# Kernel tuning notes

Hardware: AMD Instinct MI355X
Metric: run time of the kernel (lower is better)

## Reference

```python
import jax, jax.numpy as jnp
import numpy as np
import math

CH = 512
HEADS = 8
GROUPS = 32
EPS = 1e-5


def group_norm(x, w, b):
    # x: [B, C, T]
    B, C, T = x.shape
    xg = x.reshape(B, GROUPS, C // GROUPS, T)
    mu = xg.mean(axis=(2, 3), keepdims=True)
    var = xg.var(axis=(2, 3), keepdims=True)
    xg = (xg - mu) * jax.lax.rsqrt(var + EPS)
    return xg.reshape(B, C, T) * w[None, :, None] + b[None, :, None]


def conv1x1(x, w, b):
    # x: [B, C, T], w: [O, C, 1]
    return jnp.einsum('oc,bct->bot', w[:, :, 0], x) + b[None, :, None]


def conv3_same(x, w, b):
    y = jax.lax.conv_general_dilated(x, w, window_strides=(1,), padding='SAME',
                                     dimension_numbers=('NCH', 'OIH', 'NCH'))
    return y + b[None, :, None]


def setup_inputs() -> dict:
    key = jax.random.key(0)
    ks = jax.random.split(key, 12)
    B, Ti, Ts = 2, 4096, 1024
    inp = {
        'image': jax.random.normal(ks[0], (B, Ti, CH), jnp.float32),
        'st': jax.random.normal(ks[1], (B, Ts, CH), jnp.float32),
        'xn_w': jnp.ones((CH,), jnp.float32),
        'xn_b': jnp.zeros((CH,), jnp.float32),
        'jn_w': jnp.ones((CH,), jnp.float32),
        'jn_b': jnp.zeros((CH,), jnp.float32),
        'xqkv_w': jax.random.normal(ks[2], (3 * CH, CH, 1), jnp.float32) * (1.0 / math.sqrt(CH)),
        'xqkv_b': jnp.zeros((3 * CH,), jnp.float32),
        'jqkv_w': jax.random.normal(ks[3], (3 * CH, CH, 1), jnp.float32) * (1.0 / math.sqrt(CH)),
        'jqkv_b': jnp.zeros((3 * CH,), jnp.float32),
        # NOTE: original zero-inits proj; we use small random weights so the
        # attention path contributes to the output (same math).
        'proj_w': jax.random.normal(ks[4], (CH, CH, 3), jnp.float32) * (0.02 / math.sqrt(3 * CH)),
        'proj_b': jnp.zeros((CH,), jnp.float32),
    }
    return inp


def reference(image, st, xn_w, xn_b, jn_w, jn_b, xqkv_w, xqkv_b, jqkv_w, jqkv_b, proj_w, proj_b):
    # image: [B, Ti, C]  st: [B, Ts, C]
    x = image.transpose(0, 2, 1)           # [B, C, Ti]
    jc = st.transpose(0, 2, 1)              # [B, C, Ts]

    x_qkv = conv1x1(group_norm(x, xn_w, xn_b), xqkv_w, xqkv_b)    # [B, 3C, Ti]
    jc_qkv = conv1x1(group_norm(jc, jn_w, jn_b), jqkv_w, jqkv_b)  # [B, 3C, Ts]

    B, _, Ti = x_qkv.shape
    ch = CH // HEADS
    scale = 1.0 / math.sqrt(math.sqrt(ch))

    img_q = x_qkv[:, :CH].reshape(B, HEADS, ch, Ti)
    st_k = jc_qkv[:, CH:2 * CH].reshape(B, HEADS, ch, -1)
    st_v = jc_qkv[:, 2 * CH:].reshape(B, HEADS, ch, -1)

    # cross-attention: image queries attend to st keys/values
    w = jnp.einsum('bhct,bhcs->bhts', img_q * scale, st_k * scale)  # [B,H,Ti,Ts]
    w = jax.nn.softmax(w.astype(jnp.float32), axis=-1).astype(w.dtype)
    attn = jnp.einsum('bhts,bhcs->bhct', w, st_v).reshape(B, CH, Ti)

    x_h = conv3_same(attn, proj_w, proj_b)
    return x + x_h  # [B, C, Ti]
```

## Files before the change

kernel.cpp:

```cpp
#include <hip/hip_runtime.h>
#include <math.h>

static constexpr int CH = 512;
static constexpr int GROUPS = 32;
static constexpr int HC = 64;
static constexpr float EPS = 1e-5f;
static constexpr int TI = 4096;
static constexpr int TS = 1024;

typedef __bf16 bf16x8 __attribute__((ext_vector_type(8)));
typedef __bf16 bf16x4 __attribute__((ext_vector_type(4)));
typedef float f32x4 __attribute__((ext_vector_type(4)));

__global__ __launch_bounds__(256) void k_gn_partial(const float* __restrict__ img,
                                                    const float* __restrict__ st,
                                                    double* __restrict__ part) {
  int bi = blockIdx.x;
  int which = bi >> 9;
  int rem = bi & 511;
  int b = rem >> 8;
  int g = (rem >> 3) & 31;
  int chunk = rem & 7;
  const float* X = which ? st : img;
  int T = which ? TS : TI;
  int rows = T >> 3;
  int tid = threadIdx.x;
  const float* base = X + ((size_t)b * T + (size_t)chunk * rows) * CH + g * 16;
  double s1 = 0.0, s2 = 0.0;
  for (int t = tid; t < rows; t += 256) {
    const float4* p = (const float4*)(base + (size_t)t * CH);
#pragma unroll
    for (int q = 0; q < 4; ++q) {
      float4 v = p[q];
      s1 += (double)v.x + (double)v.y + (double)v.z + (double)v.w;
      s2 += (double)v.x * v.x + (double)v.y * v.y + (double)v.z * v.z + (double)v.w * v.w;
    }
  }
  __shared__ double r1[256];
  __shared__ double r2[256];
  r1[tid] = s1;
  r2[tid] = s2;
  __syncthreads();
  for (int s = 128; s > 0; s >>= 1) {
    if (tid < s) { r1[tid] += r1[tid + s]; r2[tid] += r2[tid + s]; }
    __syncthreads();
  }
  if (tid == 0) {
    part[bi * 2 + 0] = r1[0];
    part[bi * 2 + 1] = r2[0];
  }
}

__global__ __launch_bounds__(128) void k_gn_final(const double* __restrict__ part,
                                                  float* __restrict__ stats_x,
                                                  float* __restrict__ stats_j) {
  int tid = threadIdx.x;
  int which = tid >> 6;
  int idx = tid & 63;
  const double* p = part + ((which << 9) + ((idx >> 5) << 8) + ((idx & 31) << 3)) * 2;
  double s1 = 0.0, s2 = 0.0;
#pragma unroll
  for (int c = 0; c < 8; ++c) {
    s1 += p[c * 2 + 0];
    s2 += p[c * 2 + 1];
  }
  int T = which ? TS : TI;
  double N = 16.0 * T;
  double mu = s1 / N;
  double var = s2 / N - mu * mu;
  float rs = (float)(1.0 / sqrt(var + (double)EPS));
  float* stats = which ? stats_j : stats_x;
  stats[idx * 2 + 0] = (float)mu;
  stats[idx * 2 + 1] = rs;
}

__global__ __launch_bounds__(256) void k_gn_apply2(const float* __restrict__ img,
                                                   const float* __restrict__ st,
                                                   const float* __restrict__ stats_x,
                                                   const float* __restrict__ stats_j,
                                                   const float* __restrict__ xn_w,
                                                   const float* __restrict__ xn_b,
                                                   const float* __restrict__ jn_w,
                                                   const float* __restrict__ jn_b,
                                                   __bf16* __restrict__ Xnp,
                                                   __bf16* __restrict__ stnp) {
  int bi = blockIdx.x;
  bool isimg = bi < 2048;
  const float* X = isimg ? img : st;
  const float* stats = isimg ? stats_x : stats_j;
  const float* nw = isimg ? xn_w : jn_w;
  const float* nb = isimg ? xn_b : jn_b;
  __bf16* Xp = isimg ? Xnp : stnp;
  int T = isimg ? TI : TS;
  size_t idx = ((size_t)(isimg ? bi : bi - 2048) * 256 + threadIdx.x) * 8;

  int b = (int)(idx / ((size_t)T * 512));
  size_t rem = idx - (size_t)b * T * 512;
  int t = (int)(rem >> 9);
  int c = (int)(rem & 511);
  int g = c >> 4;
  float mu = stats[(b * GROUPS + g) * 2 + 0];
  float rs = stats[(b * GROUPS + g) * 2 + 1];
  float4 v0 = *(const float4*)(X + idx);
  float4 v1 = *(const float4*)(X + idx + 4);
  float4 w0 = *(const float4*)(nw + c);
  float4 w1 = *(const float4*)(nw + c + 4);
  float4 q0 = *(const float4*)(nb + c);
  float4 q1 = *(const float4*)(nb + c + 4);
  float xv[8] = {v0.x, v0.y, v0.z, v0.w, v1.x, v1.y, v1.z, v1.w};
  float wv[8] = {w0.x, w0.y, w0.z, w0.w, w1.x, w1.y, w1.z, w1.w};
  float qv[8] = {q0.x, q0.y, q0.z, q0.w, q1.x, q1.y, q1.z, q1.w};
  bf16x8 r;
#pragma unroll
  for (int i = 0; i < 8; ++i) {
    float a = rs * wv[i];
    r[i] = (__bf16)fmaf(xv[i], a, qv[i] - mu * a);
  }
  size_t off = ((((size_t)b * (T >> 4) + (t >> 4)) * 16 + (c >> 5)) * 64 +
                ((c >> 3) & 3) * 16 + (t & 15)) * 8;
  *(bf16x8*)(Xp + off) = r;
}

__global__ __launch_bounds__(256) void k_pack_all(const float* __restrict__ xqkv_w,
                                                  const float* __restrict__ jqkv_w,
                                                  const float* __restrict__ proj_w,
                                                  __bf16* __restrict__ wqb,
                                                  __bf16* __restrict__ wkvb,
                                                  __bf16* __restrict__ wb3) {
  int bi = blockIdx.x;
  if (bi < 384) {
    const float* W = (bi < 128) ? xqkv_w : (jqkv_w + (size_t)CH * CH);
    __bf16* Wp = (bi < 128) ? wqb : wkvb;
    int idx = ((bi < 128) ? bi : bi - 128) * 256 + threadIdx.x;
    int lane = idx & 63;
    int l = lane & 15, g = lane >> 4;
    int cb = (idx >> 6) & 15;
    int ob = idx >> 10;
    const float* src = W + (size_t)(ob * 16 + l) * 512 + cb * 32 + g * 8;
    float4 v0 = *(const float4*)src;
    float4 v1 = *(const float4*)(src + 4);
    float xv[8] = {v0.x, v0.y, v0.z, v0.w, v1.x, v1.y, v1.z, v1.w};
    bf16x8 r;
#pragma unroll
    for (int i = 0; i < 8; ++i) r[i] = (__bf16)xv[i];
    *(bf16x8*)(Wp + (size_t)idx * 8) = r;
  } else {
    int idx = (bi - 384) * 256 + threadIdx.x;
    int lane = idx & 63;
    int l = lane & 15, g = lane >> 4;
    int ob = (idx >> 6) & 31;
    int q = idx >> 11;
    int tap = q % 3;
    int cb = q / 3;
    int o = ob * 16 + l;
    int c = cb * 32 + g * 8;
    bf16x8 r;
#pragma unroll
    for (int j = 0; j < 8; ++j) r[j] = (__bf16)proj_w[((size_t)o * 512 + c + j) * 3 + tap];
    *(bf16x8*)(wb3 + (size_t)idx * 8) = r;
  }
}

__global__ __launch_bounds__(256) void k_qkv_mfma(const __bf16* __restrict__ Xp,
                                                  const __bf16* __restrict__ Wp,
                                                  const float* __restrict__ bias,
                                                  __bf16* __restrict__ outQK,
                                                  __bf16* __restrict__ outVp,
                                                  int T) {
  int b = blockIdx.z;
  int o0 = blockIdx.y * 64;
  int tid = threadIdx.x;
  int w = tid >> 6;
  int lane = tid & 63;
  int l = lane & 15;
  int g = lane >> 4;
  int t0 = blockIdx.x * 128 + w * 32;
  int Tb = T >> 4;
  bool vmode = (outVp != nullptr) && (o0 >= 512);

  __shared__ __align__(16) __bf16 Elds[4][2048];

  f32x4 acc[2][4] = {};
  const __bf16* Xb = Xp + (size_t)b * T * 512;

  auto load_c = [&](int cb, bf16x8 (&af)[2], bf16x8 (&wf)[4]) {
#pragma unroll
    for (int m = 0; m < 2; ++m)
      af[m] = *(const bf16x8*)(Xb + ((((size_t)(t0 >> 4) + m) * 16 + cb) * 64 + lane) * 8);
#pragma unroll
    for (int n = 0; n < 4; ++n)
      wf[n] = *(const bf16x8*)(Wp + ((((size_t)(o0 >> 4) + n) * 16 + cb) * 64 + lane) * 8);
  };

  bf16x8 afA[2], wfA[4], afB[2], wfB[4];
#define QKV_LOOP(MMEXPR)                                                        \
  {                                                                             \
    load_c(0, afA, wfA);                                                        \
    _Pragma("unroll") for (int cb = 0; cb < 16; cb += 2) {                      \
      load_c(cb + 1, afB, wfB);                                                 \
      _Pragma("unroll") for (int m = 0; m < 2; ++m)                             \
          _Pragma("unroll") for (int n = 0; n < 4; ++n) {                       \
        bf16x8 af = afA[m], wf = wfA[n];                                        \
        acc[m][n] = MMEXPR;                                                     \
      }                                                                         \
      if (cb + 2 < 16) load_c(cb + 2, afA, wfA);                                \
      _Pragma("unroll") for (int m = 0; m < 2; ++m)                             \
          _Pragma("unroll") for (int n = 0; n < 4; ++n) {                       \
        bf16x8 af = afB[m], wf = wfB[n];                                        \
        acc[m][n] = MMEXPR;                                                     \
      }                                                                         \
    }                                                                           \
  }

  if (!vmode) {
    QKV_LOOP(__builtin_amdgcn_mfma_f32_16x16x32_bf16(wf, af, acc[m][n], 0, 0, 0))
    float sc = (outVp == nullptr) ? 0.125f * 1.44269504088896f : 1.0f;
    int swz = (l & 7) << 1;
    __bf16(*Eq)[64] = reinterpret_cast<__bf16(*)[64]>(&Elds[w][0]);
#pragma unroll
    for (int m = 0; m < 2; ++m)
#pragma unroll
      for (int n = 0; n < 4; ++n) {
        f32x4 bv = *(const f32x4*)(bias + o0 + 16 * n + 4 * g);
        bf16x4 pv;
#pragma unroll
        for (int r = 0; r < 4; ++r) pv[r] = (__bf16)((acc[m][n][r] + bv[r]) * sc);
        *(bf16x4*)&Eq[m * 16 + l][((4 * n + g) ^ swz) * 4] = pv;
      }
#pragma unroll
    for (int m = 0; m < 2; ++m)
#pragma unroll
      for (int cbi = 0; cbi < 2; ++cbi) {
        bf16x8 v = *(const bf16x8*)&Eq[m * 16 + l][((8 * cbi + 2 * g) ^ swz) * 4];
        *(bf16x8*)(outQK +
                   ((((size_t)b * Tb + (t0 >> 4) + m) * 16 + (o0 >> 5) + cbi) * 64 + lane) * 8) = v;
      }
  } else {
    QKV_LOOP(__builtin_amdgcn_mfma_f32_16x16x32_bf16(af, wf, acc[m][n], 0, 0, 0))
    int swzv = l & 6;
    __bf16(*Ev)[32] = reinterpret_cast<__bf16(*)[32]>(&Elds[w][0]);
#pragma unroll
    for (int m = 0; m < 2; ++m)
#pragma unroll
      for (int n = 0; n < 4; ++n) {
        float bo = bias[o0 + 16 * n + l];
        bf16x4 pv;
#pragma unroll
        for (int r = 0; r < 4; ++r) pv[r] = (__bf16)(acc[m][n][r] + bo);
        *(bf16x4*)&Ev[16 * n + l][((4 * m + g) ^ swzv) * 4] = pv;
      }
#pragma unroll
    for (int n = 0; n < 4; ++n) {
      bf16x8 v = *(const bf16x8*)&Ev[16 * n + l][((2 * g) ^ swzv) * 4];
      int cb16 = ((o0 - 512) >> 4) + n;
      *(bf16x8*)(outVp + ((((size_t)b * 32 + cb16) * 32 + (t0 >> 5)) * 64 + lane) * 8) = v;
    }
  }
#undef QKV_LOOP
}

__global__ __launch_bounds__(128, 4) void k_attn_mfma(const __bf16* __restrict__ Qp,
                                                      const __bf16* __restrict__ Kp,
                                                      const __bf16* __restrict__ Vp,
                                                      __bf16* __restrict__ outA) {
  int b = blockIdx.z;
  int h = blockIdx.y;
  int tid = threadIdx.x;
  int w = tid >> 6;
  int lane = tid & 63;
  int l = lane & 15;
  int g = lane >> 4;
  int t0 = blockIdx.x * 32;
  int swz = (l & 7) << 1;

  __shared__ __align__(16) __bf16 Pt[2][2][16][64];
  __shared__ float Ored[64][32];
  __shared__ float Lred[64][2];

  bf16x8 qf[2][2];
#pragma unroll
  for (int m = 0; m < 2; ++m)
#pragma unroll
    for (int ks = 0; ks < 2; ++ks)
      qf[m][ks] = *(const bf16x8*)(Qp + ((((size_t)b * 256 + (t0 >> 4) + m) * 16 +
                                          2 * h + ks) * 64 + lane) * 8);

  f32x4 o_acc[2][4] = {};
  float rs_acc[2] = {};

  int s_base = w * 512;
#pragma unroll 1
  for (int s0 = s_base; s0 < s_base + 512; s0 += 64) {
    bf16x8 kf[4][2];
#pragma unroll
    for (int n = 0; n < 4; ++n)
#pragma unroll
      for (int ks = 0; ks < 2; ++ks)
        kf[n][ks] = *(const bf16x8*)(Kp + ((((size_t)b * 64 + (s0 >> 4) + n) * 16 +
                                            2 * h + ks) * 64 + lane) * 8);
    bf16x8 vf[4][2];
#pragma unroll
    for (int n = 0; n < 4; ++n)
#pragma unroll
      for (int ks = 0; ks < 2; ++ks)
        vf[n][ks] = *(const bf16x8*)(Vp + ((((size_t)b * 32 + h * 4 + n) * 32 +
                                            (s0 >> 5) + ks) * 64 + lane) * 8);
    f32x4 sT[4][2];
#pragma unroll
    for (int sb = 0; sb < 4; ++sb)
#pragma unroll
      for (int tb = 0; tb < 2; ++tb) {
        f32x4 z = {0.f, 0.f, 0.f, 0.f};
        z = __builtin_amdgcn_mfma_f32_16x16x32_bf16(kf[sb][0], qf[tb][0], z, 0, 0, 0);
        sT[sb][tb] = __builtin_amdgcn_mfma_f32_16x16x32_bf16(kf[sb][1], qf[tb][1], z, 0, 0, 0);
      }
#pragma unroll
    for (int tb = 0; tb < 2; ++tb)
#pragma unroll
      for (int sb = 0; sb < 4; ++sb) {
        float p0 = exp2f(sT[sb][tb][0]);
        float p1 = exp2f(sT[sb][tb][1]);
        float p2 = exp2f(sT[sb][tb][2]);
        float p3 = exp2f(sT[sb][tb][3]);
        rs_acc[tb] += (p0 + p1) + (p2 + p3);
        bf16x4 pv;
        pv[0] = (__bf16)p0;
        pv[1] = (__bf16)p1;
        pv[2] = (__bf16)p2;
        pv[3] = (__bf16)p3;
        *(bf16x4*)&Pt[w][tb][l][((4 * sb + g) ^ swz) * 4] = pv;
      }
    bf16x8 pa[2][2];
#pragma unroll
    for (int tb = 0; tb < 2; ++tb)
#pragma unroll
      for (int ks = 0; ks < 2; ++ks)
        pa[tb][ks] = *(const bf16x8*)&Pt[w][tb][l][((8 * ks + 2 * g) ^ swz) * 4];
#pragma unroll
    for (int tb = 0; tb < 2; ++tb)
#pragma unroll
      for (int n = 0; n < 4; ++n) {
        o_acc[tb][n] = __builtin_amdgcn_mfma_f32_16x16x32_bf16(vf[n][0], pa[tb][0], o_acc[tb][n], 0, 0, 0);
        o_acc[tb][n] = __builtin_amdgcn_mfma_f32_16x16x32_bf16(vf[n][1], pa[tb][1], o_acc[tb][n], 0, 0, 0);
      }
  }

  if (w == 1) {
#pragma unroll
    for (int tb = 0; tb < 2; ++tb) {
#pragma unroll
      for (int n = 0; n < 4; ++n)
#pragma unroll
        for (int r = 0; r < 4; ++r) Ored[lane][tb * 16 + n * 4 + r] = o_acc[tb][n][r];
      Lred[lane][tb] = rs_acc[tb];
    }
  }
  __syncthreads();
  if (w == 0) {
#pragma unroll
    for (int tb = 0; tb < 2; ++tb) {
#pragma unroll
      for (int n = 0; n < 4; ++n)
#pragma unroll
        for (int r = 0; r < 4; ++r) o_acc[tb][n][r] += Ored[lane][tb * 16 + n * 4 + r];
      float v = rs_acc[tb] + Lred[lane][tb];
      v += __shfl_xor(v, 16, 64);
      v += __shfl_xor(v, 32, 64);
      float inv = 1.f / v;
#pragma unroll
      for (int n = 0; n < 4; ++n) {
        bf16x4 ov;
#pragma unroll
        for (int r = 0; r < 4; ++r) ov[r] = (__bf16)(o_acc[tb][n][r] * inv);
        *(bf16x4*)(outA + ((size_t)b * TI + t0 + 16 * tb + l) * 512 + h * 64 + 16 * n + 4 * g) = ov;
      }
    }
  }
}

__global__ __launch_bounds__(256) void k_conv3_mfma(const __bf16* __restrict__ A,
                                                    const __bf16* __restrict__ W3p,
                                                    const float* __restrict__ bias,
                                                    const float* __restrict__ image,
                                                    float* __restrict__ out) {
  int b = blockIdx.z;
  int o0 = blockIdx.y * 64;
  int ob0 = o0 >> 4;
  int tid = threadIdx.x;
  int w = tid >> 6;
  int lane = tid & 63;
  int l = lane & 15;
  int g = lane >> 4;
  int t0 = blockIdx.x * 128;
  int t0w = t0 + w * 32;

  __shared__ __align__(16) __bf16 Alds[2][130 * 32];
  __shared__ __align__(16) __bf16 Wlds[2][12 * 512];

  const __bf16* Ab = A + (size_t)b * TI * 512;

  auto stage = [&](int cb, int buf) {
#pragma unroll
    for (int pass = 0; pass < 3; ++pass) {
      int gi = tid + pass * 256;
      if (gi < 520) {
        int r = gi >> 2, gg = gi & 3;
        int t = t0 - 1 + r;
        bf16x8 v = {};
        if (t >= 0 && t < TI) v = *(const bf16x8*)(Ab + (size_t)t * 512 + cb * 32 + gg * 8);
        *(bf16x8*)&Alds[buf][r * 32 + ((gg ^ (r & 3)) << 3)] = v;
      }
    }
#pragma unroll
    for (int ch = w; ch < 12; ch += 4) {
      bf16x8 v = *(const bf16x8*)(W3p + ((((size_t)cb * 3 + (ch >> 2)) * 32 + ob0 +
                                          (ch & 3)) * 64 + lane) * 8);
      *(bf16x8*)&Wlds[buf][ch * 512 + lane * 8] = v;
    }
  };

  f32x4 acc[2][4] = {};

  stage(0, 0);
  __syncthreads();
#pragma unroll 1
  for (int cs = 0; cs < 16; ++cs) {
    int cur = cs & 1;
    if (cs < 15) stage(cs + 1, cur ^ 1);
    bf16x8 af[3][2], wf[3][4];
#pragma unroll
    for (int tap = 0; tap < 3; ++tap) {
#pragma unroll
      for (int m = 0; m < 2; ++m) {
        int r = w * 32 + 16 * m + l + tap;
        af[tap][m] = *(const bf16x8*)&Alds[cur][r * 32 + ((g ^ (r & 3)) << 3)];
      }
#pragma unroll
      for (int n = 0; n < 4; ++n)
        wf[tap][n] = *(const bf16x8*)&Wlds[cur][(tap * 4 + n) * 512 + lane * 8];
    }
#pragma unroll
    for (int tap = 0; tap < 3; ++tap)
#pragma unroll
      for (int m = 0; m < 2; ++m)
#pragma unroll
        for (int n = 0; n < 4; ++n)
          acc[m][n] =
              __builtin_amdgcn_mfma_f32_16x16x32_bf16(af[tap][m], wf[tap][n], acc[m][n], 0, 0, 0);
    __syncthreads();
  }

#pragma unroll
  for (int m = 0; m < 2; ++m) {
    int tb = t0w + 16 * m + 4 * g;
#pragma unroll
    for (int n = 0; n < 4; ++n) {
      int o = o0 + 16 * n + l;
      float bo = bias[o];
      f32x4 r;
#pragma unroll
      for (int rr = 0; rr < 4; ++rr)
        r[rr] = acc[m][n][rr] + bo + image[((size_t)b * TI + tb + rr) * CH + o];
      *(f32x4*)(out + ((size_t)b * CH + o) * TI + tb) = r;
    }
  }
}

extern "C" void kernel_launch(void* const* d_in, const int* in_sizes, int n_in,
                              void* d_out, int out_size, void* d_ws, size_t ws_size,
                              hipStream_t stream) {
  const float* image = (const float*)d_in[0];
  const float* st = (const float*)d_in[1];
  const float* xn_w = (const float*)d_in[2];
  const float* xn_b = (const float*)d_in[3];
  const float* jn_w = (const float*)d_in[4];
  const float* jn_b = (const float*)d_in[5];
  const float* xqkv_w = (const float*)d_in[6];
  const float* xqkv_b = (const float*)d_in[7];
  const float* jqkv_w = (const float*)d_in[8];
  const float* jqkv_b = (const float*)d_in[9];
  const float* proj_w = (const float*)d_in[10];
  const float* proj_b = (const float*)d_in[11];
  float* out = (float*)d_out;
  float* ws = (float*)d_ws;

  double* part = (double*)ws;
  float* stats_x = ws + 4096;
  float* stats_j = ws + 4096 + 128;
  __bf16* Xnp = (__bf16*)(ws + 4096 + 256);
  __bf16* abuf = Xnp;
  __bf16* stnp = Xnp + (size_t)2 * TI * CH;
  __bf16* wqb = stnp + (size_t)2 * TS * CH;
  __bf16* wkvb = wqb + (size_t)CH * CH;
  __bf16* wb3 = wkvb + (size_t)2 * CH * CH;
  __bf16* Qp = wb3 + (size_t)3 * CH * CH;
  __bf16* Kp = Qp + (size_t)2 * TI * CH;
  __bf16* Vp = Kp + (size_t)2 * TS * CH;

  k_gn_partial<<<dim3(1024), dim3(256), 0, stream>>>(image, st, part);
  k_gn_final<<<dim3(1), dim3(128), 0, stream>>>(part, stats_x, stats_j);

  k_gn_apply2<<<dim3(2560), dim3(256), 0, stream>>>(image, st, stats_x, stats_j,
                                                    xn_w, xn_b, jn_w, jn_b, Xnp, stnp);

  k_pack_all<<<dim3(768), dim3(256), 0, stream>>>(xqkv_w, jqkv_w, proj_w, wqb, wkvb, wb3);

  k_qkv_mfma<<<dim3(TI / 128, CH / 64, 2), dim3(256), 0, stream>>>(
      Xnp, wqb, xqkv_b, Qp, nullptr, TI);
  k_qkv_mfma<<<dim3(TS / 128, 1024 / 64, 2), dim3(256), 0, stream>>>(
      stnp, wkvb, jqkv_b + CH, Kp, Vp, TS);

  k_attn_mfma<<<dim3(TI / 32, 8, 2), dim3(128), 0, stream>>>(Qp, Kp, Vp, abuf);

  k_conv3_mfma<<<dim3(TI / 128, CH / 64, 2), dim3(256), 0, stream>>>(
      abuf, wb3, proj_b, image, out);
}
```

Measured before the change: 117.2 us.

## Software-pipeline attention loop with double-buffered K fragments and P tiles

The attention kernel's S loop now handles two 64-key tiles per iteration. The next K fragments are prefetched into a second register set while the current QK^T and softmax run. The P staging buffer in LDS is doubled so the PV MFMAs of one tile can interleave with the softmax stores of the next, and s_setprio raises wave priority around the MFMA blocks. The separate Ored reduction buffer now aliases the second half of Pt to keep LDS use down, and launch bounds drop the minimum blocks per SM from 4 to 3 to make room for the extra registers, at the cost of lower occupancy.

```diff
diff --git a/kernel.cpp b/kernel.cpp
--- a/kernel.cpp
+++ b/kernel.cpp
@@ -259,7 +259,7 @@
 #undef QKV_LOOP
 }
 
-__global__ __launch_bounds__(128, 4) void k_attn_mfma(const __bf16* __restrict__ Qp,
+__global__ __launch_bounds__(128, 3) void k_attn_mfma(const __bf16* __restrict__ Qp,
                                                       const __bf16* __restrict__ Kp,
                                                       const __bf16* __restrict__ Vp,
                                                       __bf16* __restrict__ outA) {
@@ -273,9 +273,9 @@
   int t0 = blockIdx.x * 32;
   int swz = (l & 7) << 1;
 
-  __shared__ __align__(16) __bf16 Pt[2][2][16][64];
-  __shared__ float Ored[64][32];
+  __shared__ __align__(16) __bf16 Pt[2][2][2][16][64];
   __shared__ float Lred[64][2];
+  float* OredP = (float*)&Pt[1][0][0][0][0];
 
   bf16x8 qf[2][2];
 #pragma unroll
@@ -287,25 +287,26 @@
 
   f32x4 o_acc[2][4] = {};
   float rs_acc[2] = {};
-
-  int s_base = w * 512;
-#pragma unroll 1
-  for (int s0 = s_base; s0 < s_base + 512; s0 += 64) {
-    bf16x8 kf[4][2];
+  bf16x8 kf0[4][2], kf1[4][2], vf[4][2];
+
+  auto load_k = [&](int s0, bf16x8 (&kf)[4][2]) {
 #pragma unroll
     for (int n = 0; n < 4; ++n)
 #pragma unroll
       for (int ks = 0; ks < 2; ++ks)
         kf[n][ks] = *(const bf16x8*)(Kp + ((((size_t)b * 64 + (s0 >> 4) + n) * 16 +
                                             2 * h + ks) * 64 + lane) * 8);
-    bf16x8 vf[4][2];
+  };
+  auto load_v = [&](int s0) {
 #pragma unroll
     for (int n = 0; n < 4; ++n)
 #pragma unroll
       for (int ks = 0; ks < 2; ++ks)
         vf[n][ks] = *(const bf16x8*)(Vp + ((((size_t)b * 32 + h * 4 + n) * 32 +
                                             (s0 >> 5) + ks) * 64 + lane) * 8);
-    f32x4 sT[4][2];
+  };
+  auto qk = [&](bf16x8 (&kf)[4][2], f32x4 (&sT)[4][2]) {
+    __builtin_amdgcn_s_setprio(1);
 #pragma unroll
     for (int sb = 0; sb < 4; ++sb)
 #pragma unroll
@@ -314,6 +315,9 @@
         z = __builtin_amdgcn_mfma_f32_16x16x32_bf16(kf[sb][0], qf[tb][0], z, 0, 0, 0);
         sT[sb][tb] = __builtin_amdgcn_mfma_f32_16x16x32_bf16(kf[sb][1], qf[tb][1], z, 0, 0, 0);
       }
+    __builtin_amdgcn_s_setprio(0);
+  };
+  auto softmax_store = [&](f32x4 (&sT)[4][2], int ab) {
 #pragma unroll
     for (int tb = 0; tb < 2; ++tb)
 #pragma unroll
@@ -328,14 +332,17 @@
         pv[1] = (__bf16)p1;
         pv[2] = (__bf16)p2;
         pv[3] = (__bf16)p3;
-        *(bf16x4*)&Pt[w][tb][l][((4 * sb + g) ^ swz) * 4] = pv;
-      }
+        *(bf16x4*)&Pt[w][ab][tb][l][((4 * sb + g) ^ swz) * 4] = pv;
+      }
+  };
+  auto pv_acc = [&](int ab) {
     bf16x8 pa[2][2];
 #pragma unroll
     for (int tb = 0; tb < 2; ++tb)
 #pragma unroll
       for (int ks = 0; ks < 2; ++ks)
-        pa[tb][ks] = *(const bf16x8*)&Pt[w][tb][l][((8 * ks + 2 * g) ^ swz) * 4];
+        pa[tb][ks] = *(const bf16x8*)&Pt[w][ab][tb][l][((8 * ks + 2 * g) ^ swz) * 4];
+    __builtin_amdgcn_s_setprio(1);
 #pragma unroll
     for (int tb = 0; tb < 2; ++tb)
 #pragma unroll
@@ -343,6 +350,24 @@
         o_acc[tb][n] = __builtin_amdgcn_mfma_f32_16x16x32_bf16(vf[n][0], pa[tb][0], o_acc[tb][n], 0, 0, 0);
         o_acc[tb][n] = __builtin_amdgcn_mfma_f32_16x16x32_bf16(vf[n][1], pa[tb][1], o_acc[tb][n], 0, 0, 0);
       }
+    __builtin_amdgcn_s_setprio(0);
+  };
+
+  int sbeg = w * 512;
+  load_k(sbeg, kf0);
+#pragma unroll 1
+  for (int s0 = sbeg; s0 < sbeg + 512; s0 += 128) {
+    f32x4 sT[4][2];
+    load_v(s0);
+    load_k(s0 + 64, kf1);
+    qk(kf0, sT);
+    softmax_store(sT, 0);
+    qk(kf1, sT);
+    pv_acc(0);
+    load_v(s0 + 64);
+    if (s0 + 128 < sbeg + 512) load_k(s0 + 128, kf0);
+    softmax_store(sT, 1);
+    pv_acc(1);
   }
 
   if (w == 1) {
@@ -351,7 +376,7 @@
 #pragma unroll
       for (int n = 0; n < 4; ++n)
 #pragma unroll
-        for (int r = 0; r < 4; ++r) Ored[lane][tb * 16 + n * 4 + r] = o_acc[tb][n][r];
+        for (int r = 0; r < 4; ++r) OredP[lane * 32 + tb * 16 + n * 4 + r] = o_acc[tb][n][r];
       Lred[lane][tb] = rs_acc[tb];
     }
   }
@@ -362,7 +387,7 @@
 #pragma unroll
       for (int n = 0; n < 4; ++n)
 #pragma unroll
-        for (int r = 0; r < 4; ++r) o_acc[tb][n][r] += Ored[lane][tb * 16 + n * 4 + r];
+        for (int r = 0; r < 4; ++r) o_acc[tb][n][r] += OredP[lane * 32 + tb * 16 + n * 4 + r];
       float v = rs_acc[tb] + Lred[lane][tb];
       v += __shfl_xor(v, 16, 64);
       v += __shfl_xor(v, 32, 64);
```

New measurement: 176.7 us. +50.8%, slower.
